# Kernel tuning notes

Hardware: AMD Instinct MI355X
Metric: run time of the kernel (lower is better)

Reference implementation:

```python
import jax, jax.numpy as jnp
import numpy as np

N_NODES = 100000
N_EDGES = 1600000
N_GRAPHS = 256
D_IN = 128
D_HID = 128
D_OUT = 7
BN_EPS = 1e-5


def setup_inputs() -> dict:
    key = jax.random.key(0)
    ks = jax.random.split(key, 16)
    def lin(k, fan_in, fan_out):
        # torch.nn.Linear init: U(-1/sqrt(fan_in), 1/sqrt(fan_in)); stored as [in, out]
        bound = 1.0 / np.sqrt(fan_in)
        kw, kb = jax.random.split(k)
        w = jax.random.uniform(kw, (fan_in, fan_out), jnp.float32, -bound, bound)
        b = jax.random.uniform(kb, (fan_out,), jnp.float32, -bound, bound)
        return w, b
    x = jax.random.normal(ks[0], (N_NODES, D_IN), jnp.float32)
    edge_index = jax.random.randint(ks[1], (2, N_EDGES), 0, N_NODES, jnp.int64)
    batch = jnp.sort(jax.random.randint(ks[2], (N_NODES,), 0, N_GRAPHS, jnp.int64))
    w1a, b1a = lin(ks[3], D_IN, D_HID)
    w1b, b1b = lin(ks[4], D_HID, D_HID)
    w2a, b2a = lin(ks[5], D_HID, D_HID)
    w2b, b2b = lin(ks[6], D_HID, D_HID)
    wl, bl = lin(ks[7], D_HID, D_OUT)
    g1 = jnp.ones((D_HID,), jnp.float32); be1 = jnp.zeros((D_HID,), jnp.float32)
    g2 = jnp.ones((D_HID,), jnp.float32); be2 = jnp.zeros((D_HID,), jnp.float32)
    return {"x": x, "w1a": w1a, "b1a": b1a, "w1b": w1b, "b1b": b1b,
            "g1": g1, "be1": be1,
            "w2a": w2a, "b2a": b2a, "w2b": w2b, "b2b": b2b,
            "g2": g2, "be2": be2,
            "wl": wl, "bl": bl,
            "edge_index": edge_index, "batch": batch}


def gin_conv(x, edge_index, wa, ba, wb, bb):
    src, dst = edge_index[0], edge_index[1]
    # sum aggregation of source features at target nodes (eps = 0)
    agg = jax.ops.segment_sum(x[src], dst, num_segments=N_NODES)
    h = x + agg
    h = jnp.maximum(h @ wa + ba, 0.0)
    return h @ wb + bb


def batch_norm(x, gamma, beta):
    mean = jnp.mean(x, axis=0)
    var = jnp.mean(jnp.square(x - mean), axis=0)  # biased, training-mode stats
    return (x - mean) * (gamma / jnp.sqrt(var + BN_EPS)) + beta


def reference(x, w1a, b1a, w1b, b1b, g1, be1,
              w2a, b2a, w2b, b2b, g2, be2,
              wl, bl, edge_index, batch):
    h = gin_conv(x, edge_index, w1a, b1a, w1b, b1b)
    h = jnp.maximum(batch_norm(h, g1, be1), 0.0)
    h = gin_conv(h, edge_index, w2a, b2a, w2b, b2b)
    h = jnp.maximum(batch_norm(h, g2, be2), 0.0)
    # global mean pool over graphs
    sums = jax.ops.segment_sum(h, batch, num_segments=N_GRAPHS)
    cnts = jax.ops.segment_sum(jnp.ones((h.shape[0],), h.dtype), batch, num_segments=N_GRAPHS)
    pooled = sums / jnp.maximum(cnts, 1.0)[:, None]  # [G, D_HID]
    logits = pooled @ wl + bl
    return jax.nn.log_softmax(logits, axis=1)
```

## Files before the change

kernel.cpp:

```cpp
#include <hip/hip_runtime.h>
#include <math.h>

#define NN 100000
#define NE 1600000
#define NG 256
#define D 128
#define EPS 1e-5f
#define MAXDEG 64
#define EPB 12800
#define SLICE_N 12500
#define GRID_FILL 1000
#define GRID_CAST 6250
#define GRID_TW 32
#define GRID_GEMM 782

typedef __attribute__((ext_vector_type(8))) short s16x8;
typedef __attribute__((ext_vector_type(4))) float f32x4;
typedef __attribute__((ext_vector_type(4))) float f32x4v;
typedef __attribute__((ext_vector_type(4))) uint u32x4;

__device__ __forceinline__ ushort f2b(float f) {
    uint u = __float_as_uint(f);
    uint r = (u + 0x7fffu + ((u >> 16) & 1u)) >> 16;
    return (ushort)r;
}
__device__ __forceinline__ float blo(uint u) { return __uint_as_float(u << 16); }
__device__ __forceinline__ float bhi(uint u) { return __uint_as_float(u & 0xFFFF0000u); }

#define SWZW(lin) ((lin) ^ ((((lin) >> 8) & 7) << 4))

__global__ __launch_bounds__(256) void prep(const int* __restrict__ esrc, const int* __restrict__ edst,
                                            int* __restrict__ cursor, int* __restrict__ slots,
                                            const float* __restrict__ x, ushort* __restrict__ xb,
                                            const float* __restrict__ w1a, const float* __restrict__ w1b,
                                            const float* __restrict__ w2a, const float* __restrict__ w2b,
                                            ushort* __restrict__ Wt) {
    int b = blockIdx.x;
    if (b < GRID_FILL) {
        const int slice = b & 7;
        const int chunk = b >> 3;
        const int lo = slice * SLICE_N, hi = lo + SLICE_N;
        const int ebase = chunk * EPB;
        for (int i = threadIdx.x; i < EPB / 4; i += 256) {
            int e = ebase + i * 4;
            int4 s = *(const int4*)(esrc + e);
            int4 d = *(const int4*)(edst + e);
            if (d.x >= lo && d.x < hi) { int p = atomicAdd(&cursor[d.x], 1); slots[(d.x << 6) | (p & 63)] = s.x; }
            if (d.y >= lo && d.y < hi) { int p = atomicAdd(&cursor[d.y], 1); slots[(d.y << 6) | (p & 63)] = s.y; }
            if (d.z >= lo && d.z < hi) { int p = atomicAdd(&cursor[d.z], 1); slots[(d.z << 6) | (p & 63)] = s.z; }
            if (d.w >= lo && d.w < hi) { int p = atomicAdd(&cursor[d.w], 1); slots[(d.w << 6) | (p & 63)] = s.w; }
        }
    } else if (b < GRID_FILL + GRID_CAST) {
        int i = (b - GRID_FILL) * 256 + threadIdx.x;
        if (i * 8 < NN * D) {
            f32x4v v0 = __builtin_nontemporal_load((const f32x4v*)(x + i * 8));
            f32x4v v1 = __builtin_nontemporal_load((const f32x4v*)(x + i * 8) + 1);
            ushort o[8] = {f2b(v0.x), f2b(v0.y), f2b(v0.z), f2b(v0.w),
                           f2b(v1.x), f2b(v1.y), f2b(v1.z), f2b(v1.w)};
            __builtin_nontemporal_store(*(u32x4*)o, (u32x4*)(xb + i * 8));
        }
    } else {
        int by = b - GRID_FILL - GRID_CAST;
        int wsel = by >> 3, bx = by & 7;
        const float* W = (wsel == 0) ? w1a : (wsel == 1) ? w1b : (wsel == 2) ? w2a : w2b;
        ushort* T = Wt + wsel * 16384;
        for (int i = bx * 256 + threadIdx.x; i < 16384; i += 8 * 256) {
            int k = i >> 7, cc = i & 127;
            T[(cc << 7) | k] = f2b(W[i]);
        }
    }
}

template <int FUSE_BN>
__global__ __launch_bounds__(256) void gather_slots(ushort* __restrict__ out, const ushort* __restrict__ feat,
                                                    const int* __restrict__ deg, const int* __restrict__ slots,
                                                    const float* __restrict__ scale, const float* __restrict__ shift) {
    int node = __builtin_amdgcn_readfirstlane(blockIdx.x * 4 + (threadIdx.x >> 6));
    if (node >= NN) return;
    int lane = threadIdx.x & 63;
    int n = deg[node];
    n = (n > MAXDEG) ? MAXDEG : n;
    const int* sl = slots + (node << 6);
    float scx = 1.f, scy = 1.f, shx = 0.f, shy = 0.f;
    if (FUSE_BN) {
        float2 sc = *(const float2*)(scale + lane * 2);
        float2 sh = *(const float2*)(shift + lane * 2);
        scx = sc.x; scy = sc.y; shx = sh.x; shy = sh.y;
    }
    uint ub = *(const uint*)(feat + node * D + lane * 2);
    float axv[8], ayv[8];
#pragma unroll
    for (int j = 0; j < 8; ++j) { axv[j] = 0.f; ayv[j] = 0.f; }
    if (FUSE_BN) {
        axv[0] = fmaxf(fmaf(blo(ub), scx, shx), 0.f);
        ayv[0] = fmaxf(fmaf(bhi(ub), scy, shy), 0.f);
    } else {
        axv[0] = blo(ub); ayv[0] = bhi(ub);
    }
    int e = 0;
    for (; e + 15 < n; e += 16) {
        uint u[16];
#pragma unroll
        for (int j = 0; j < 16; ++j) u[j] = *(const uint*)(feat + sl[e + j] * D + lane * 2);
#pragma unroll
        for (int j = 0; j < 16; ++j) {
            int j8 = j & 7;
            if (FUSE_BN) {
                axv[j8] += fmaxf(fmaf(blo(u[j]), scx, shx), 0.f);
                ayv[j8] += fmaxf(fmaf(bhi(u[j]), scy, shy), 0.f);
            } else {
                axv[j8] += blo(u[j]); ayv[j8] += bhi(u[j]);
            }
        }
    }
    for (; e + 7 < n; e += 8) {
        uint u[8];
#pragma unroll
        for (int j = 0; j < 8; ++j) u[j] = *(const uint*)(feat + sl[e + j] * D + lane * 2);
#pragma unroll
        for (int j = 0; j < 8; ++j) {
            if (FUSE_BN) {
                axv[j] += fmaxf(fmaf(blo(u[j]), scx, shx), 0.f);
                ayv[j] += fmaxf(fmaf(bhi(u[j]), scy, shy), 0.f);
            } else {
                axv[j] += blo(u[j]); ayv[j] += bhi(u[j]);
            }
        }
    }
    for (; e + 3 < n; e += 4) {
        uint u[4];
#pragma unroll
        for (int j = 0; j < 4; ++j) u[j] = *(const uint*)(feat + sl[e + j] * D + lane * 2);
#pragma unroll
        for (int j = 0; j < 4; ++j) {
            if (FUSE_BN) {
                axv[j] += fmaxf(fmaf(blo(u[j]), scx, shx), 0.f);
                ayv[j] += fmaxf(fmaf(bhi(u[j]), scy, shy), 0.f);
            } else {
                axv[j] += blo(u[j]); ayv[j] += bhi(u[j]);
            }
        }
    }
    for (; e < n; ++e) {
        uint u0 = *(const uint*)(feat + sl[e] * D + lane * 2);
        if (FUSE_BN) {
            axv[0] += fmaxf(fmaf(blo(u0), scx, shx), 0.f);
            ayv[0] += fmaxf(fmaf(bhi(u0), scy, shy), 0.f);
        } else {
            axv[0] += blo(u0); ayv[0] += bhi(u0);
        }
    }
    float ax = ((axv[0] + axv[1]) + (axv[2] + axv[3])) + ((axv[4] + axv[5]) + (axv[6] + axv[7]));
    float ay = ((ayv[0] + ayv[1]) + (ayv[2] + ayv[3])) + ((ayv[4] + ayv[5]) + (ayv[6] + ayv[7]));
    uint o = (uint)f2b(ax) | ((uint)f2b(ay) << 16);
    *(uint*)(out + node * D + lane * 2) = o;
}

__global__ __launch_bounds__(512, 4) void gemm_dual(const ushort* __restrict__ G,
                                                    const ushort* __restrict__ Wta, const float* __restrict__ ba,
                                                    const ushort* __restrict__ Wtb, const float* __restrict__ bb,
                                                    ushort* __restrict__ H, float4* __restrict__ stat, int nrows) {
    __shared__ ushort wbuf[16384];
    __shared__ ushort tbuf[16384];
    __shared__ float4 red[8][64];
    char* wb = (char*)wbuf;
    char* tb = (char*)tbuf;

    const int tid = threadIdx.x;
    const int lane = tid & 63;
    const int wave = tid >> 6;
    const int lr = lane & 15;
    const int kg = lane >> 4;
    const int rloc = wave * 16 + lr;
    const int grow = blockIdx.x * 128 + rloc;
    const int growc = (grow > nrows - 1) ? (nrows - 1) : grow;
    const int wrow = lr * 256;
    const int wswz = (lr & 7) << 4;

    const ushort* gp = G + growc * D + kg * 8;
    s16x8 af0 = *(const s16x8*)(gp);
    s16x8 af1 = *(const s16x8*)(gp + 32);
    s16x8 af2 = *(const s16x8*)(gp + 64);
    s16x8 af3 = *(const s16x8*)(gp + 96);

#pragma unroll
    for (int i = 0; i < 4; ++i) {
        int lin = i * 8192 + tid * 16;
        uint4 v = *(const uint4*)((const char*)Wta + lin);
        *(uint4*)(wb + SWZW(lin)) = v;
    }
    __syncthreads();

    f32x4 acc[8];
#pragma unroll
    for (int ct = 0; ct < 8; ++ct) acc[ct] = (f32x4)0.f;

#pragma unroll
    for (int ks = 0; ks < 4; ++ks) {
        s16x8 af = (ks == 0) ? af0 : (ks == 1) ? af1 : (ks == 2) ? af2 : af3;
        const int wofs = (kg * 16 + ks * 64) ^ wswz;
#pragma unroll
        for (int ct = 0; ct < 8; ++ct) {
            s16x8 a = *(const s16x8*)(wb + wrow + ct * 4096 + wofs);
            acc[ct] = __builtin_amdgcn_mfma_f32_16x16x32_bf16(a, af, acc[ct], 0, 0, 0);
        }
    }

#pragma unroll
    for (int ct = 0; ct < 8; ++ct) {
        int k0 = ct * 16 + kg * 4;
        float4 bv = *(const float4*)(ba + k0);
        float o0 = fmaxf(acc[ct][0] + bv.x, 0.f);
        float o1 = fmaxf(acc[ct][1] + bv.y, 0.f);
        float o2 = fmaxf(acc[ct][2] + bv.z, 0.f);
        float o3 = fmaxf(acc[ct][3] + bv.w, 0.f);
        ushort pk[4] = {f2b(o0), f2b(o1), f2b(o2), f2b(o3)};
        int kb = k0 >> 3;
        int off = ((k0 >> 5) << 13) | ((kb & 3) << 11) | ((rloc ^ (kb & 7)) << 4) | ((k0 & 7) << 1);
        *(uint2*)(tb + off) = *(const uint2*)pk;
    }
    __syncthreads();

#pragma unroll
    for (int i = 0; i < 4; ++i) {
        int lin = i * 8192 + tid * 16;
        uint4 v = *(const uint4*)((const char*)Wtb + lin);
        *(uint4*)(wb + SWZW(lin)) = v;
    }
    s16x8 bf[4];
#pragma unroll
    for (int ks = 0; ks < 4; ++ks) {
        int kb = ks * 4 + kg;
        bf[ks] = *(const s16x8*)(tb + ((ks << 13) | (kg << 11) | ((rloc ^ (kb & 7)) << 4)));
    }
    __syncthreads();

#pragma unroll
    for (int ct = 0; ct < 8; ++ct) acc[ct] = (f32x4)0.f;
#pragma unroll
    for (int ks = 0; ks < 4; ++ks) {
        const int wofs = (kg * 16 + ks * 64) ^ wswz;
#pragma unroll
        for (int ct = 0; ct < 8; ++ct) {
            s16x8 a = *(const s16x8*)(wb + wrow + ct * 4096 + wofs);
            acc[ct] = __builtin_amdgcn_mfma_f32_16x16x32_bf16(a, bf[ks], acc[ct], 0, 0, 0);
        }
    }

#pragma unroll
    for (int ct = 0; ct < 8; ++ct) {
        int k0 = ct * 16 + kg * 4;
        float4 bv = *(const float4*)(bb + k0);
        uint2 pk2 = make_uint2(0u, 0u);
        if (grow < nrows) {
            float o0 = acc[ct][0] + bv.x;
            float o1 = acc[ct][1] + bv.y;
            float o2 = acc[ct][2] + bv.z;
            float o3 = acc[ct][3] + bv.w;
            ushort pk[4] = {f2b(o0), f2b(o1), f2b(o2), f2b(o3)};
            pk2 = *(const uint2*)pk;
            *(uint2*)(H + grow * D + k0) = pk2;
        }
        int kb = k0 >> 3;
        int off = ((k0 >> 5) << 13) | ((kb & 3) << 11) | ((rloc ^ (kb & 7)) << 4) | ((k0 & 7) << 1);
        *(uint2*)(tb + off) = pk2;
    }
    __syncthreads();

    {
        int c2 = tid & 63;
        int rg = tid >> 6;
        int k = c2 * 2;
        int kb = k >> 3;
        int base = ((k >> 5) << 13) | ((kb & 3) << 11) | ((k & 7) << 1);
        float s0 = 0.f, q0 = 0.f, s1 = 0.f, q1 = 0.f;
#pragma unroll 4
        for (int i = 0; i < 16; ++i) {
            int row = rg * 16 + i;
            uint u = *(const uint*)(tb + base + ((row ^ (kb & 7)) << 4));
            float lo = blo(u), hi = bhi(u);
            s0 += lo; q0 += lo * lo; s1 += hi; q1 += hi * hi;
        }
        red[rg][c2] = make_float4(s0, q0, s1, q1);
    }
    __syncthreads();
    if (tid < 64) {
        float4 r0 = red[0][tid], r1 = red[1][tid], r2 = red[2][tid], r3 = red[3][tid];
        float4 r4 = red[4][tid], r5 = red[5][tid], r6 = red[6][tid], r7 = red[7][tid];
        float4 o;
        o.x = ((r0.x + r1.x) + (r2.x + r3.x)) + ((r4.x + r5.x) + (r6.x + r7.x));
        o.y = ((r0.y + r1.y) + (r2.y + r3.y)) + ((r4.y + r5.y) + (r6.y + r7.y));
        o.z = ((r0.z + r1.z) + (r2.z + r3.z)) + ((r4.z + r5.z) + (r6.z + r7.z));
        o.w = ((r0.w + r1.w) + (r2.w + r3.w)) + ((r4.w + r5.w) + (r6.w + r7.w));
        stat[blockIdx.x * 64 + tid] = o;
    }
}

__global__ __launch_bounds__(256) void bn_reduce(const float4* __restrict__ stat, int nblk,
                                                 const float* __restrict__ gamma, const float* __restrict__ beta,
                                                 float* __restrict__ scale, float* __restrict__ shift, int nrows) {
    const int f4 = blockIdx.x;
    const int t = threadIdx.x;
    float s0 = 0.f, q0 = 0.f, s1 = 0.f, q1 = 0.f;
    for (int b = t; b < nblk; b += 256) {
        float4 v = stat[b * 64 + f4];
        s0 += v.x; q0 += v.y; s1 += v.z; q1 += v.w;
    }
    __shared__ float4 red[256];
    red[t] = make_float4(s0, q0, s1, q1);
    __syncthreads();
    for (int off = 128; off >= 1; off >>= 1) {
        if (t < off) {
            float4 a = red[t], b = red[t + off];
            red[t] = make_float4(a.x + b.x, a.y + b.y, a.z + b.z, a.w + b.w);
        }
        __syncthreads();
    }
    if (t == 0) {
        float4 v = red[0];
        int f0 = 2 * f4, f1 = 2 * f4 + 1;
        double m0 = (double)v.x / nrows, var0 = (double)v.y / nrows - m0 * m0;
        double m1 = (double)v.z / nrows, var1 = (double)v.w / nrows - m1 * m1;
        float sc0 = gamma[f0] * rsqrtf((float)var0 + EPS);
        float sc1 = gamma[f1] * rsqrtf((float)var1 + EPS);
        scale[f0] = sc0; shift[f0] = beta[f0] - (float)m0 * sc0;
        scale[f1] = sc1; shift[f1] = beta[f1] - (float)m1 * sc1;
    }
}

__global__ __launch_bounds__(256) void pool_partial(const ushort* __restrict__ h, const int* __restrict__ batch,
                                                    const float* __restrict__ scale, const float* __restrict__ shift,
                                                    float* __restrict__ pooled) {
    int wave = threadIdx.x >> 6;
    int lane = threadIdx.x & 63;
    int r0 = blockIdx.x * 256 + wave * 64;
    if (r0 >= NN) return;
    int f2 = lane * 2;
    float2 sc = *(const float2*)(scale + f2);
    float2 sh = *(const float2*)(shift + f2);
    float ax = 0.f, ay = 0.f;
    int cur = -1;
    int rend = r0 + 64; if (rend > NN) rend = NN;
    for (int r = r0; r < rend; ++r) {
        int g = batch[r];
        if (g != cur) {
            if (cur >= 0) {
                atomicAdd(&pooled[cur * D + f2], ax);
                atomicAdd(&pooled[cur * D + f2 + 1], ay);
            }
            cur = g; ax = 0.f; ay = 0.f;
        }
        uint u = *(const uint*)(h + r * D + f2);
        ax += fmaxf(fmaf(blo(u), sc.x, sh.x), 0.f);
        ay += fmaxf(fmaf(bhi(u), sc.y, sh.y), 0.f);
    }
    if (cur >= 0) {
        atomicAdd(&pooled[cur * D + f2], ax);
        atomicAdd(&pooled[cur * D + f2 + 1], ay);
    }
}

__device__ __forceinline__ int lower_bound_i(const int* a, int n, int v) {
    int lo = 0, hi = n;
    while (lo < hi) {
        int m = (lo + hi) >> 1;
        if (a[m] < v) lo = m + 1; else hi = m;
    }
    return lo;
}

__global__ __launch_bounds__(256) void head(const float* __restrict__ pooled, const int* __restrict__ batch,
                                            const float* __restrict__ wl, const float* __restrict__ bl,
                                            float* __restrict__ out) {
    int g = blockIdx.x * 256 + threadIdx.x;
    if (g >= NG) return;
    int lo = lower_bound_i(batch, NN, g);
    int hi = lower_bound_i(batch, NN, g + 1);
    float inv = 1.f / fmaxf((float)(hi - lo), 1.f);
    float logits[7];
#pragma unroll
    for (int c = 0; c < 7; ++c) logits[c] = bl[c];
    for (int k = 0; k < D; ++k) {
        float p = pooled[g * D + k] * inv;
#pragma unroll
        for (int c = 0; c < 7; ++c) logits[c] = fmaf(p, wl[k * 7 + c], logits[c]);
    }
    float m = logits[0];
#pragma unroll
    for (int c = 1; c < 7; ++c) m = fmaxf(m, logits[c]);
    float s = 0.f;
#pragma unroll
    for (int c = 0; c < 7; ++c) s += expf(logits[c] - m);
    float lse = m + logf(s);
#pragma unroll
    for (int c = 0; c < 7; ++c) out[g * 7 + c] = logits[c] - lse;
}

extern "C" void kernel_launch(void* const* d_in, const int* in_sizes, int n_in,
                              void* d_out, int out_size, void* d_ws, size_t ws_size,
                              hipStream_t stream) {
    const float* x   = (const float*)d_in[0];
    const float* w1a = (const float*)d_in[1];
    const float* b1a = (const float*)d_in[2];
    const float* w1b = (const float*)d_in[3];
    const float* b1b = (const float*)d_in[4];
    const float* g1  = (const float*)d_in[5];
    const float* be1 = (const float*)d_in[6];
    const float* w2a = (const float*)d_in[7];
    const float* b2a = (const float*)d_in[8];
    const float* w2b = (const float*)d_in[9];
    const float* b2b = (const float*)d_in[10];
    const float* g2  = (const float*)d_in[11];
    const float* be2 = (const float*)d_in[12];
    const float* wl  = (const float*)d_in[13];
    const float* bl  = (const float*)d_in[14];
    const int* ei    = (const int*)d_in[15];
    const int* batch = (const int*)d_in[16];
    float* out = (float*)d_out;

    const int* esrc = ei;
    const int* edst = ei + NE;

    char* ws = (char*)d_ws;
    ushort* B0 = (ushort*)(ws);
    ushort* B1 = (ushort*)(ws + 25600000);
    ushort* B2 = (ushort*)(ws + 51200000);
    int* slots   = (int*)(ws + 76800000);
    int* cursor  = (int*)(ws + 102400000);
    float* pooled = (float*)(ws + 102800000);
    float* scale1 = (float*)(ws + 102931072);
    float* shift1 = scale1 + 128;
    float* scale2 = shift1 + 128;
    float* shift2 = scale2 + 128;
    ushort* Wt    = (ushort*)(ws + 102933120);
    float4* stat  = (float4*)(ws + 103064192);
    ushort* Wt1a = Wt, *Wt1b = Wt + 16384, *Wt2a = Wt + 32768, *Wt2b = Wt + 49152;

    const int grid_prep = GRID_FILL + GRID_CAST + GRID_TW;
    const int grid_stat = (NN + 255) / 256;
    const int grid_gath = (NN + 3) / 4;

    hipMemsetAsync(cursor, 0, 531072, stream);

    prep<<<grid_prep, 256, 0, stream>>>(esrc, edst, cursor, slots, x, B0, w1a, w1b, w2a, w2b, Wt);

    gather_slots<0><<<grid_gath, 256, 0, stream>>>(B1, B0, cursor, slots, nullptr, nullptr);
    gemm_dual<<<GRID_GEMM, 512, 0, stream>>>(B1, Wt1a, b1a, Wt1b, b1b, B2, stat, NN);
    bn_reduce<<<64, 256, 0, stream>>>(stat, GRID_GEMM, g1, be1, scale1, shift1, NN);

    gather_slots<1><<<grid_gath, 256, 0, stream>>>(B0, B2, cursor, slots, scale1, shift1);
    gemm_dual<<<GRID_GEMM, 512, 0, stream>>>(B0, Wt2a, b2a, Wt2b, b2b, B1, stat, NN);
    bn_reduce<<<64, 256, 0, stream>>>(stat, GRID_GEMM, g2, be2, scale2, shift2, NN);

    pool_partial<<<grid_stat, 256, 0, stream>>>(B1, batch, scale2, shift2, pooled);
    head<<<1, 256, 0, stream>>>(pooled, batch, wl, bl, out);
}
```

Baseline: 310.6 us.

## Replace sliced global-atomic CSR fill with two-pass binned counting sort

Edge slot construction changes from 1000 blocks that each scan an edge chunk filtered by destination slice and use global atomics per edge, to two passes. The first pass buckets packed (local dst, src) pairs into 196 bins using LDS atomics and one global atomic per bin per tile. The second pass drains each bin with LDS cursors to fill the slots and write degrees. This removes the 8x redundant edge reads and per-edge global atomics, at the cost of an extra kernel launch and a binbuf round trip. Bins are capped at 12288 entries, so edges beyond that are silently dropped. The x cast also loses its nontemporal hints.

```diff
diff --git a/kernel.cpp b/kernel.cpp
--- a/kernel.cpp
+++ b/kernel.cpp
@@ -7,17 +7,17 @@
 #define D 128
 #define EPS 1e-5f
 #define MAXDEG 64
-#define EPB 12800
-#define SLICE_N 12500
-#define GRID_FILL 1000
+#define NBINS 196
+#define BINSZ 512
+#define BINCAP 12288
+#define GRID_BIN 125
+#define EPB_A 12800
 #define GRID_CAST 6250
 #define GRID_TW 32
 #define GRID_GEMM 782
 
 typedef __attribute__((ext_vector_type(8))) short s16x8;
 typedef __attribute__((ext_vector_type(4))) float f32x4;
-typedef __attribute__((ext_vector_type(4))) float f32x4v;
-typedef __attribute__((ext_vector_type(4))) uint u32x4;
 
 __device__ __forceinline__ ushort f2b(float f) {
     uint u = __float_as_uint(f);
@@ -29,38 +29,58 @@
 
 #define SWZW(lin) ((lin) ^ ((((lin) >> 8) & 7) << 4))
 
-__global__ __launch_bounds__(256) void prep(const int* __restrict__ esrc, const int* __restrict__ edst,
-                                            int* __restrict__ cursor, int* __restrict__ slots,
-                                            const float* __restrict__ x, ushort* __restrict__ xb,
-                                            const float* __restrict__ w1a, const float* __restrict__ w1b,
-                                            const float* __restrict__ w2a, const float* __restrict__ w2b,
-                                            ushort* __restrict__ Wt) {
+__global__ __launch_bounds__(256) void prep1(const int* __restrict__ esrc, const int* __restrict__ edst,
+                                             uint* __restrict__ binbuf, int* __restrict__ bincnt,
+                                             const float* __restrict__ x, ushort* __restrict__ xb,
+                                             const float* __restrict__ w1a, const float* __restrict__ w1b,
+                                             const float* __restrict__ w2a, const float* __restrict__ w2b,
+                                             ushort* __restrict__ Wt) {
     int b = blockIdx.x;
-    if (b < GRID_FILL) {
-        const int slice = b & 7;
-        const int chunk = b >> 3;
-        const int lo = slice * SLICE_N, hi = lo + SLICE_N;
-        const int ebase = chunk * EPB;
-        for (int i = threadIdx.x; i < EPB / 4; i += 256) {
-            int e = ebase + i * 4;
-            int4 s = *(const int4*)(esrc + e);
-            int4 d = *(const int4*)(edst + e);
-            if (d.x >= lo && d.x < hi) { int p = atomicAdd(&cursor[d.x], 1); slots[(d.x << 6) | (p & 63)] = s.x; }
-            if (d.y >= lo && d.y < hi) { int p = atomicAdd(&cursor[d.y], 1); slots[(d.y << 6) | (p & 63)] = s.y; }
-            if (d.z >= lo && d.z < hi) { int p = atomicAdd(&cursor[d.z], 1); slots[(d.z << 6) | (p & 63)] = s.z; }
-            if (d.w >= lo && d.w < hi) { int p = atomicAdd(&cursor[d.w], 1); slots[(d.w << 6) | (p & 63)] = s.w; }
-        }
-    } else if (b < GRID_FILL + GRID_CAST) {
-        int i = (b - GRID_FILL) * 256 + threadIdx.x;
+    if (b < GRID_BIN) {
+        __shared__ int cnt[NBINS], lbase[NBINS];
+        const int ebase = b * EPB_A;
+        for (int it = 0; it < 13; ++it) {
+            for (int t = threadIdx.x; t < NBINS; t += 256) cnt[t] = 0;
+            __syncthreads();
+            int e = ebase + it * 1024 + threadIdx.x * 4;
+            bool valid = (e < ebase + EPB_A);
+            int4 s = make_int4(0, 0, 0, 0), d = make_int4(0, 0, 0, 0);
+            if (valid) {
+                s = *(const int4*)(esrc + e);
+                d = *(const int4*)(edst + e);
+            }
+            int b0 = d.x >> 9, b1 = d.y >> 9, b2 = d.z >> 9, b3 = d.w >> 9;
+            int o0 = 0, o1 = 0, o2 = 0, o3 = 0;
+            if (valid) {
+                o0 = atomicAdd(&cnt[b0], 1);
+                o1 = atomicAdd(&cnt[b1], 1);
+                o2 = atomicAdd(&cnt[b2], 1);
+                o3 = atomicAdd(&cnt[b3], 1);
+            }
+            __syncthreads();
+            for (int t = threadIdx.x; t < NBINS; t += 256)
+                lbase[t] = (cnt[t] > 0) ? atomicAdd(&bincnt[t], cnt[t]) : 0;
+            __syncthreads();
+            if (valid) {
+                uint p0 = (uint)(lbase[b0] + o0), p1 = (uint)(lbase[b1] + o1);
+                uint p2 = (uint)(lbase[b2] + o2), p3 = (uint)(lbase[b3] + o3);
+                if (p0 < BINCAP) binbuf[b0 * BINCAP + p0] = ((uint)(d.x & 511) << 17) | (uint)s.x;
+                if (p1 < BINCAP) binbuf[b1 * BINCAP + p1] = ((uint)(d.y & 511) << 17) | (uint)s.y;
+                if (p2 < BINCAP) binbuf[b2 * BINCAP + p2] = ((uint)(d.z & 511) << 17) | (uint)s.z;
+                if (p3 < BINCAP) binbuf[b3 * BINCAP + p3] = ((uint)(d.w & 511) << 17) | (uint)s.w;
+            }
+        }
+    } else if (b < GRID_BIN + GRID_CAST) {
+        int i = (b - GRID_BIN) * 256 + threadIdx.x;
         if (i * 8 < NN * D) {
-            f32x4v v0 = __builtin_nontemporal_load((const f32x4v*)(x + i * 8));
-            f32x4v v1 = __builtin_nontemporal_load((const f32x4v*)(x + i * 8) + 1);
+            float4 v0 = *(const float4*)(x + i * 8);
+            float4 v1 = *(const float4*)(x + i * 8 + 4);
             ushort o[8] = {f2b(v0.x), f2b(v0.y), f2b(v0.z), f2b(v0.w),
                            f2b(v1.x), f2b(v1.y), f2b(v1.z), f2b(v1.w)};
-            __builtin_nontemporal_store(*(u32x4*)o, (u32x4*)(xb + i * 8));
+            *(uint4*)(xb + i * 8) = *(uint4*)o;
         }
     } else {
-        int by = b - GRID_FILL - GRID_CAST;
+        int by = b - GRID_BIN - GRID_CAST;
         int wsel = by >> 3, bx = by & 7;
         const float* W = (wsel == 0) ? w1a : (wsel == 1) ? w1b : (wsel == 2) ? w2a : w2b;
         ushort* T = Wt + wsel * 16384;
@@ -69,6 +89,42 @@
             T[(cc << 7) | k] = f2b(W[i]);
         }
     }
+}
+
+__global__ __launch_bounds__(256) void drain(const uint* __restrict__ binbuf, const int* __restrict__ bincnt,
+                                             int* __restrict__ deg, int* __restrict__ slots) {
+    const int bin = blockIdx.x;
+    int n = bincnt[bin]; if (n > BINCAP) n = BINCAP;
+    __shared__ int cur[BINSZ];
+    cur[threadIdx.x] = 0;
+    cur[threadIdx.x + 256] = 0;
+    __syncthreads();
+    const uint* bp = binbuf + bin * BINCAP;
+    const int base = bin << 9;
+    int i = threadIdx.x;
+    for (; i + 768 < n; i += 1024) {
+        uint u0 = bp[i], u1 = bp[i + 256], u2 = bp[i + 512], u3 = bp[i + 768];
+        int l0 = u0 >> 17, l1 = u1 >> 17, l2 = u2 >> 17, l3 = u3 >> 17;
+        int p0 = atomicAdd(&cur[l0], 1);
+        int p1 = atomicAdd(&cur[l1], 1);
+        int p2 = atomicAdd(&cur[l2], 1);
+        int p3 = atomicAdd(&cur[l3], 1);
+        slots[((base + l0) << 6) | (p0 & 63)] = (int)(u0 & 0x1FFFFu);
+        slots[((base + l1) << 6) | (p1 & 63)] = (int)(u1 & 0x1FFFFu);
+        slots[((base + l2) << 6) | (p2 & 63)] = (int)(u2 & 0x1FFFFu);
+        slots[((base + l3) << 6) | (p3 & 63)] = (int)(u3 & 0x1FFFFu);
+    }
+    for (; i < n; i += 256) {
+        uint u0 = bp[i];
+        int l0 = u0 >> 17;
+        int p0 = atomicAdd(&cur[l0], 1);
+        slots[((base + l0) << 6) | (p0 & 63)] = (int)(u0 & 0x1FFFFu);
+    }
+    __syncthreads();
+    int node = base + threadIdx.x;
+    if (node < NN) deg[node] = cur[threadIdx.x];
+    node += 256;
+    if (node < NN) deg[node] = cur[threadIdx.x + 256];
 }
 
 template <int FUSE_BN>
@@ -425,30 +481,33 @@
     ushort* B0 = (ushort*)(ws);
     ushort* B1 = (ushort*)(ws + 25600000);
     ushort* B2 = (ushort*)(ws + 51200000);
+    uint* binbuf = (uint*)(ws + 25600000);
     int* slots   = (int*)(ws + 76800000);
-    int* cursor  = (int*)(ws + 102400000);
-    float* pooled = (float*)(ws + 102800000);
-    float* scale1 = (float*)(ws + 102931072);
+    int* deg     = (int*)(ws + 102400000);
+    int* bincnt  = (int*)(ws + 102800000);
+    float* pooled = (float*)(ws + 102801024);
+    float* scale1 = (float*)(ws + 102932096);
     float* shift1 = scale1 + 128;
     float* scale2 = shift1 + 128;
     float* shift2 = scale2 + 128;
-    ushort* Wt    = (ushort*)(ws + 102933120);
-    float4* stat  = (float4*)(ws + 103064192);
+    ushort* Wt    = (ushort*)(ws + 102934144);
+    float4* stat  = (float4*)(ws + 103065216);
     ushort* Wt1a = Wt, *Wt1b = Wt + 16384, *Wt2a = Wt + 32768, *Wt2b = Wt + 49152;
 
-    const int grid_prep = GRID_FILL + GRID_CAST + GRID_TW;
+    const int grid_prep = GRID_BIN + GRID_CAST + GRID_TW;
     const int grid_stat = (NN + 255) / 256;
     const int grid_gath = (NN + 3) / 4;
 
-    hipMemsetAsync(cursor, 0, 531072, stream);
-
-    prep<<<grid_prep, 256, 0, stream>>>(esrc, edst, cursor, slots, x, B0, w1a, w1b, w2a, w2b, Wt);
-
-    gather_slots<0><<<grid_gath, 256, 0, stream>>>(B1, B0, cursor, slots, nullptr, nullptr);
+    hipMemsetAsync(bincnt, 0, 132096, stream);
+
+    prep1<<<grid_prep, 256, 0, stream>>>(esrc, edst, binbuf, bincnt, x, B0, w1a, w1b, w2a, w2b, Wt);
+    drain<<<NBINS, 256, 0, stream>>>(binbuf, bincnt, deg, slots);
+
+    gather_slots<0><<<grid_gath, 256, 0, stream>>>(B1, B0, deg, slots, nullptr, nullptr);
     gemm_dual<<<GRID_GEMM, 512, 0, stream>>>(B1, Wt1a, b1a, Wt1b, b1b, B2, stat, NN);
     bn_reduce<<<64, 256, 0, stream>>>(stat, GRID_GEMM, g1, be1, scale1, shift1, NN);
 
-    gather_slots<1><<<grid_gath, 256, 0, stream>>>(B0, B2, cursor, slots, scale1, shift1);
+    gather_slots<1><<<grid_gath, 256, 0, stream>>>(B0, B2, deg, slots, scale1, shift1);
     gemm_dual<<<GRID_GEMM, 512, 0, stream>>>(B0, Wt2a, b2a, Wt2b, b2b, B1, stat, NN);
     bn_reduce<<<64, 256, 0, stream>>>(stat, GRID_GEMM, g2, be2, scale2, shift2, NN);
 
```

New measurement: 290.0 us. 6.7% less time.
